# Optimization experiments

Measured on AMD Instinct MI355X. Metric: run time of the kernel, lower is better.

Reference implementation:

```python
import jax, jax.numpy as jnp
import numpy as np

B, N, K, D = 4, 2048, 32, 256
TOKEN_DIM = 256
EGO_DIM = 256
NUM_HEADS = 4
LN_EPS = 1e-6


def masked_softmax(logits, mask, axis):
    mask = mask.astype(jnp.bool_)
    while mask.ndim < logits.ndim:
        mask = mask[..., None]
    neg_big = jnp.finfo(logits.dtype).min
    has_any = jnp.any(mask, axis=axis, keepdims=True)
    masked_logits = jnp.where(mask, logits, neg_big)
    masked_logits = jnp.where(has_any, masked_logits, 0.0)
    weights = jax.nn.softmax(masked_logits, axis=axis)
    weights = jnp.where(mask, weights, 0.0)
    denom = jnp.sum(weights, axis=axis, keepdims=True)
    weights = jnp.where(denom > 0, weights / denom, 0.0)
    return weights


def setup_inputs() -> dict:
    key = jax.random.key(0)
    ks = jax.random.split(key, 10)
    inv_tok = jax.random.normal(ks[0], (B, N, K, D), dtype=jnp.float32)
    ego_ctx = jax.random.normal(ks[1], (B, N, EGO_DIM), dtype=jnp.float32)
    r = jax.random.normal(ks[2], (B, N, K, 3), dtype=jnp.float32)
    u = jax.random.normal(ks[3], (B, N, K, 3), dtype=jnp.float32)
    mask = jax.random.randint(ks[4], (B, N, K), 0, 2).astype(jnp.bool_)
    # params
    W_ego = jax.random.normal(ks[5], (EGO_DIM, TOKEN_DIM), dtype=jnp.float32) * 0.05
    b_ego = jnp.zeros((TOKEN_DIM,), dtype=jnp.float32)
    ln_scale = jnp.ones((D,), dtype=jnp.float32)
    ln_bias = jnp.zeros((D,), dtype=jnp.float32)
    W_h = jax.random.normal(ks[6], (D + TOKEN_DIM, TOKEN_DIM), dtype=jnp.float32) * 0.05
    b_h = jnp.zeros((TOKEN_DIM,), dtype=jnp.float32)
    W_logit = jax.random.normal(ks[7], (TOKEN_DIM, NUM_HEADS), dtype=jnp.float32) * 0.01
    b_logit = jnp.zeros((NUM_HEADS,), dtype=jnp.float32)
    return {"inv_tok": inv_tok, "ego_ctx": ego_ctx, "r": r, "u": u, "mask": mask,
            "W_ego": W_ego, "b_ego": b_ego, "ln_scale": ln_scale, "ln_bias": ln_bias,
            "W_h": W_h, "b_h": b_h, "W_logit": W_logit, "b_logit": b_logit}


def reference(inv_tok, ego_ctx, r, u, mask, W_ego, b_ego, ln_scale, ln_bias, W_h, b_h, W_logit, b_logit):
    # ego context projection, broadcast over K
    ego_h = ego_ctx @ W_ego + b_ego                      # (B,N,T)
    ego_b = jnp.broadcast_to(ego_h[:, :, None, :], (B, N, K, TOKEN_DIM))
    # LayerNorm over last axis of inv_tok
    mean = jnp.mean(inv_tok, axis=-1, keepdims=True)
    var = jnp.var(inv_tok, axis=-1, keepdims=True)
    ln = (inv_tok - mean) * jax.lax.rsqrt(var + LN_EPS) * ln_scale + ln_bias
    h = jnp.concatenate([ln, ego_b], axis=-1)            # (B,N,K,D+T)
    h = jax.nn.gelu(h @ W_h + b_h, approximate=True)     # (B,N,K,T)
    logits = h @ W_logit + b_logit                       # (B,N,K,H)
    alpha = masked_softmax(logits, mask, axis=-2)        # (B,N,K,H)
    v_r = jnp.einsum('bnkh,bnkd->bnhd', alpha, r).reshape(B, N, 3 * NUM_HEADS)
    v_u = jnp.einsum('bnkh,bnkd->bnhd', alpha, u).reshape(B, N, 3 * NUM_HEADS)
    return (v_r, v_u, alpha)
```

## Files before the change

kernel.cpp:

```cpp
#include <hip/hip_runtime.h>

#define BN_TOTAL 8192
#define KTOK 32
#define DDIM 256
#define TDIM 256

typedef float f32x4 __attribute__((ext_vector_type(4)));
typedef short bf16x8 __attribute__((ext_vector_type(8)));

__device__ __forceinline__ unsigned short f2bf(float f){
    unsigned int u = __builtin_bit_cast(unsigned int, f);
    u = u + 0x7fffu + ((u >> 16) & 1u);
    return (unsigned short)(u >> 16);
}
__device__ __forceinline__ float bf2f(unsigned short h){
    unsigned int u = ((unsigned int)h) << 16;
    return __builtin_bit_cast(float, u);
}
__device__ __forceinline__ float gelu_tanh(float x){
    float y = 1.5957691216057308f * (x + 0.044715f * x * x * x);
    return x / (1.0f + __expf(-y));
}

__device__ __forceinline__ int packpos(int k, int n, int NT){
    int kt = k >> 5, quad = (k >> 3) & 3, j = k & 7;
    int nt = n >> 4, nl = n & 15;
    return ((kt * NT + nt) * 64 + quad * 16 + nl) * 8 + j;
}

__global__ __launch_bounds__(256) void pack_weights(const float* __restrict__ Wh,
        const float* __restrict__ Wlogit, const float* __restrict__ b_ego,
        const float* __restrict__ b_h,
        unsigned short* __restrict__ Bp1, unsigned short* __restrict__ BpL,
        float* __restrict__ b_combo){
    int bid = blockIdx.x, tid = threadIdx.x;
    if (bid < 64){
        int base = (bid * 256 + tid) * 4;
        for (int e = base; e < base + 4; ++e){
            int k = e >> 8, n = e & 255;
            Bp1[packpos(k, n, 16)] = f2bf(Wh[k * 256 + n]);
        }
    } else if (bid == 64){
        for (int e = tid * 16; e < tid * 16 + 16; ++e){
            int k = e >> 4, n = e & 15;
            float v = (n < 4) ? Wlogit[k * 4 + n] : 0.0f;
            BpL[packpos(k, n, 1)] = f2bf(v);
        }
    } else {
        float acc = b_h[tid];
        for (int j = 0; j < 256; ++j) acc += b_ego[j] * Wh[(256 + j) * 256 + tid];
        b_combo[tid] = acc;
    }
}

__global__ __launch_bounds__(256) void combo_pack(const float* __restrict__ Wego,
        const float* __restrict__ Wh, unsigned short* __restrict__ Bpc){
    __shared__ float row[256];
    int k = blockIdx.x, n = threadIdx.x;
    row[n] = Wego[k * 256 + n];
    __syncthreads();
    float acc = 0.f;
    const float4* row4 = (const float4*)row;
    for (int j4 = 0; j4 < 64; ++j4){
        float4 e = row4[j4];
        int j = j4 * 4;
        acc += e.x * Wh[(256 + j) * 256 + n];
        acc += e.y * Wh[(257 + j) * 256 + n];
        acc += e.z * Wh[(258 + j) * 256 + n];
        acc += e.w * Wh[(259 + j) * 256 + n];
    }
    Bpc[packpos(k, n, 16)] = f2bf(acc);
}

__global__ __launch_bounds__(256) void ego_gemm(const float* __restrict__ ego_ctx,
        const unsigned short* __restrict__ Bpc, const float* __restrict__ b_combo,
        unsigned short* __restrict__ ego_term){
    int w = threadIdx.x >> 6, l = threadIdx.x & 63;
    int row = blockIdx.x * 64 + w * 16 + (l & 15);
    f32x4 acc[16];
    #pragma unroll
    for (int i = 0; i < 16; ++i) acc[i] = 0;
    #pragma unroll
    for (int kt = 0; kt < 8; ++kt){
        int k0 = kt * 32 + ((l >> 4) << 3);
        const float* ap = ego_ctx + row * 256 + k0;
        float4 x0 = *(const float4*)ap;
        float4 x1 = *(const float4*)(ap + 4);
        bf16x8 a;
        a[0]=(short)f2bf(x0.x); a[1]=(short)f2bf(x0.y); a[2]=(short)f2bf(x0.z); a[3]=(short)f2bf(x0.w);
        a[4]=(short)f2bf(x1.x); a[5]=(short)f2bf(x1.y); a[6]=(short)f2bf(x1.z); a[7]=(short)f2bf(x1.w);
        #pragma unroll
        for (int nt = 0; nt < 16; ++nt){
            bf16x8 b = *(const bf16x8*)&Bpc[((kt * 16 + nt) * 64 + l) * 8];
            acc[nt] = __builtin_amdgcn_mfma_f32_16x16x32_bf16(a, b, acc[nt], 0, 0, 0);
        }
    }
    int rq = (l >> 4) * 4, col = l & 15;
    int rbase = blockIdx.x * 64 + w * 16 + rq;
    #pragma unroll
    for (int nt = 0; nt < 16; ++nt){
        int n = nt * 16 + col;
        float bc = b_combo[n];
        #pragma unroll
        for (int rg = 0; rg < 4; ++rg)
            ego_term[(rbase + rg) * 256 + n] = f2bf(acc[nt][rg] + bc);
    }
}

__global__ __launch_bounds__(256) void main_fused(const float* __restrict__ inv,
        const float* __restrict__ rin, const float* __restrict__ uin,
        const int* __restrict__ mask, const float* __restrict__ ln_s,
        const float* __restrict__ ln_b, const float* __restrict__ b_logit,
        const unsigned short* __restrict__ Bp1, const unsigned short* __restrict__ BpL,
        const unsigned short* __restrict__ ego_term, float* __restrict__ out){

    __shared__ unsigned short Albs[64 * 264];
    __shared__ float ego_s[2][256];
    __shared__ float logit_s[64 * 4];
    __shared__ float alpha_s[64 * 4];

    int tid = threadIdx.x;
    int w = tid >> 6, l = tid & 63;
    int T0 = blockIdx.x * 64;
    int bn0 = blockIdx.x * 2;

    for (int i = tid; i < 512; i += 256)
        ego_s[i >> 8][i & 255] = bf2f(ego_term[bn0 * 256 + i]);

    {
        float4 sc = *(const float4*)&ln_s[l * 4];
        float4 bs = *(const float4*)&ln_b[l * 4];
        int r0 = w * 16;
        const float* base = inv + (T0 + r0) * 256 + l * 4;
        float4 cur = *(const float4*)base;
        #pragma unroll
        for (int rr = 0; rr < 16; ++rr){
            float4 nxt = cur;
            if (rr < 15) nxt = *(const float4*)(base + (rr + 1) * 256);
            float s  = cur.x + cur.y + cur.z + cur.w;
            float s2 = cur.x*cur.x + cur.y*cur.y + cur.z*cur.z + cur.w*cur.w;
            #pragma unroll
            for (int off = 32; off >= 1; off >>= 1){
                s  += __shfl_xor(s,  off);
                s2 += __shfl_xor(s2, off);
            }
            float mean = s * (1.0f / 256.0f);
            float var  = s2 * (1.0f / 256.0f) - mean * mean;
            float rstd = rsqrtf(var + 1e-6f);
            ushort4 o;
            o.x = f2bf((cur.x - mean) * rstd * sc.x + bs.x);
            o.y = f2bf((cur.y - mean) * rstd * sc.y + bs.y);
            o.z = f2bf((cur.z - mean) * rstd * sc.z + bs.z);
            o.w = f2bf((cur.w - mean) * rstd * sc.w + bs.w);
            *(ushort4*)&Albs[(r0 + rr) * 264 + l * 4] = o;
            cur = nxt;
        }
    }
    __syncthreads();

    f32x4 acc[4][4];
    #pragma unroll
    for (int a = 0; a < 4; ++a)
        #pragma unroll
        for (int b = 0; b < 4; ++b) acc[a][b] = 0;
    {
        int kq = (l >> 4) << 3, ml = l & 15;
        #pragma unroll
        for (int kt = 0; kt < 8; ++kt){
            int ko = kt * 32 + kq;
            bf16x8 af[4], bfv[4];
            #pragma unroll
            for (int mt = 0; mt < 4; ++mt)
                af[mt] = *(const bf16x8*)&Albs[(mt * 16 + ml) * 264 + ko];
            #pragma unroll
            for (int i = 0; i < 4; ++i)
                bfv[i] = *(const bf16x8*)&Bp1[((kt * 16 + (w * 4 + i)) * 64 + l) * 8];
            #pragma unroll
            for (int mt = 0; mt < 4; ++mt)
                #pragma unroll
                for (int i = 0; i < 4; ++i)
                    acc[mt][i] = __builtin_amdgcn_mfma_f32_16x16x32_bf16(af[mt], bfv[i], acc[mt][i], 0, 0, 0);
        }
    }
    __syncthreads();

    {
        int col = l & 15, rq = (l >> 4) * 4;
        #pragma unroll
        for (int mt = 0; mt < 4; ++mt){
            int g = mt >> 1;
            #pragma unroll
            for (int i = 0; i < 4; ++i){
                int n = (w * 4 + i) * 16 + col;
                float eg = ego_s[g][n];
                #pragma unroll
                for (int rg = 0; rg < 4; ++rg){
                    float x = acc[mt][i][rg] + eg;
                    Albs[(mt * 16 + rq + rg) * 264 + n] = f2bf(gelu_tanh(x));
                }
            }
        }
    }
    __syncthreads();

    {
        int kq = (l >> 4) << 3, ml = l & 15;
        f32x4 lacc = 0;
        #pragma unroll
        for (int kt = 0; kt < 8; ++kt){
            bf16x8 a = *(const bf16x8*)&Albs[(w * 16 + ml) * 264 + kt * 32 + kq];
            bf16x8 b = *(const bf16x8*)&BpL[(kt * 64 + l) * 8];
            lacc = __builtin_amdgcn_mfma_f32_16x16x32_bf16(a, b, lacc, 0, 0, 0);
        }
        if (ml < 4){
            float bl = b_logit[ml];
            int rq = (l >> 4) * 4;
            #pragma unroll
            for (int rg = 0; rg < 4; ++rg)
                logit_s[(w * 16 + rq + rg) * 4 + ml] = lacc[rg] + bl;
        }
    }
    __syncthreads();

    {
        int g = w >> 1;
        int h = ((w & 1) << 1) + (l >> 5);
        int k = l & 31;
        int valid = mask[T0 + g * 32 + k] != 0;
        float lg = logit_s[(g * 32 + k) * 4 + h];
        float val = valid ? lg : -3.0e38f;
        float mx = val;
        #pragma unroll
        for (int off = 16; off >= 1; off >>= 1)
            mx = fmaxf(mx, __shfl_xor(mx, off));
        float e = valid ? __expf(lg - mx) : 0.0f;
        float ssum = e;
        #pragma unroll
        for (int off = 16; off >= 1; off >>= 1)
            ssum += __shfl_xor(ssum, off);
        float a = (ssum > 0.f) ? e / ssum : 0.0f;
        alpha_s[(g * 32 + k) * 4 + h] = a;
        out[196608 + (T0 + g * 32 + k) * 4 + h] = a;
    }
    __syncthreads();

    if (tid < 48){
        int g = tid / 24, rem = tid % 24;
        int which = rem / 12, hd = rem % 12;
        int h = hd / 3, d = hd % 3;
        const float* src = which ? uin : rin;
        const float* sp = src + (T0 + g * 32) * 3 + d;
        float acc2 = 0.f;
        #pragma unroll
        for (int k = 0; k < 32; ++k)
            acc2 += alpha_s[(g * 32 + k) * 4 + h] * sp[k * 3];
        out[which * 98304 + (bn0 + g) * 12 + hd] = acc2;
    }
}

extern "C" void kernel_launch(void* const* d_in, const int* in_sizes, int n_in,
                              void* d_out, int out_size, void* d_ws, size_t ws_size,
                              hipStream_t stream){
    const float* inv    = (const float*)d_in[0];
    const float* ego    = (const float*)d_in[1];
    const float* rin    = (const float*)d_in[2];
    const float* uin    = (const float*)d_in[3];
    const int*   mask   = (const int*)  d_in[4];
    const float* Wego   = (const float*)d_in[5];
    const float* b_ego  = (const float*)d_in[6];
    const float* ln_s   = (const float*)d_in[7];
    const float* ln_b   = (const float*)d_in[8];
    const float* Wh     = (const float*)d_in[9];
    const float* b_h    = (const float*)d_in[10];
    const float* Wlogit = (const float*)d_in[11];
    const float* b_lg   = (const float*)d_in[12];
    float* out = (float*)d_out;

    unsigned short* wsu = (unsigned short*)d_ws;
    unsigned short* Bp1 = wsu;
    unsigned short* Bpc = wsu + 65536;
    unsigned short* BpL = wsu + 131072;
    float* b_combo      = (float*)(wsu + 135168);
    unsigned short* ego_term = wsu + 135680;

    pack_weights<<<66, 256, 0, stream>>>(Wh, Wlogit, b_ego, b_h, Bp1, BpL, b_combo);
    combo_pack<<<256, 256, 0, stream>>>(Wego, Wh, Bpc);
    ego_gemm<<<128, 256, 0, stream>>>(ego, Bpc, b_combo, ego_term);
    main_fused<<<4096, 256, 0, stream>>>(inv, rin, uin, mask, ln_s, ln_b, b_lg,
                                         Bp1, BpL, ego_term, out);
}
```

Baseline: 473.9 us.

## Fold LayerNorm into GEMM epilogue via MFMA-computed row statistics

LayerNorm is no longer applied before the GEMM. Raw inv_tok is packed to bf16 directly, and the LN scale is folded into the packed Wh weights. The LN bias is folded into the combined bias, and a precomputed column-sum vector v1 handles the mean correction. Per-row sum and sum of squares are produced by extra MFMAs (against a ones vector and against the row itself), and normalisation is applied in the GELU epilogue. This removes the shuffle-reduction pass from the load phase. The prep kernels are merged into one launch, ego_gemm is re-tiled across more blocks, and GELU uses a hardware reciprocal. The cost is precision: statistics come from bf16-rounded inputs and the variance uses the E[x^2]-mean^2 form.

```diff
diff --git a/kernel.cpp b/kernel.cpp
--- a/kernel.cpp
+++ b/kernel.cpp
@@ -1,9 +1,4 @@
 #include <hip/hip_runtime.h>
-
-#define BN_TOTAL 8192
-#define KTOK 32
-#define DDIM 256
-#define TDIM 256
 
 typedef float f32x4 __attribute__((ext_vector_type(4)));
 typedef short bf16x8 __attribute__((ext_vector_type(8)));
@@ -17,9 +12,15 @@
     unsigned int u = ((unsigned int)h) << 16;
     return __builtin_bit_cast(float, u);
 }
-__device__ __forceinline__ float gelu_tanh(float x){
-    float y = 1.5957691216057308f * (x + 0.044715f * x * x * x);
-    return x / (1.0f + __expf(-y));
+__device__ __forceinline__ unsigned int pk2(float a, float b){
+    return (unsigned int)f2bf(a) | ((unsigned int)f2bf(b) << 16);
+}
+__device__ __forceinline__ float gelu_f(float x){
+    float t = x * x;
+    float u = fmaf(0.044715f, t, 1.0f);
+    float y = 1.5957691216057308f * x * u;
+    float e = __expf(-y);
+    return x * __builtin_amdgcn_rcpf(1.0f + e);
 }
 
 __device__ __forceinline__ int packpos(int k, int n, int NT){
@@ -28,17 +29,22 @@
     return ((kt * NT + nt) * 64 + quad * 16 + nl) * 8 + j;
 }
 
-__global__ __launch_bounds__(256) void pack_weights(const float* __restrict__ Wh,
-        const float* __restrict__ Wlogit, const float* __restrict__ b_ego,
-        const float* __restrict__ b_h,
+__global__ __launch_bounds__(256) void prep(const float* __restrict__ Wh,
+        const float* __restrict__ Wlogit, const float* __restrict__ Wego,
+        const float* __restrict__ b_ego, const float* __restrict__ b_h,
+        const float* __restrict__ ln_s, const float* __restrict__ ln_b,
         unsigned short* __restrict__ Bp1, unsigned short* __restrict__ BpL,
-        float* __restrict__ b_combo){
+        unsigned short* __restrict__ Bpc, float* __restrict__ b_combo,
+        float* __restrict__ v1){
+    __shared__ float rowbuf[256];
     int bid = blockIdx.x, tid = threadIdx.x;
     if (bid < 64){
         int base = (bid * 256 + tid) * 4;
+        int k = base >> 8;
+        float sc = ln_s[k];
         for (int e = base; e < base + 4; ++e){
-            int k = e >> 8, n = e & 255;
-            Bp1[packpos(k, n, 16)] = f2bf(Wh[k * 256 + n]);
+            int n = e & 255;
+            Bp1[packpos(k, n, 16)] = f2bf(sc * Wh[k * 256 + n]);
         }
     } else if (bid == 64){
         for (int e = tid * 16; e < tid * 16 + 16; ++e){
@@ -46,157 +52,167 @@
             float v = (n < 4) ? Wlogit[k * 4 + n] : 0.0f;
             BpL[packpos(k, n, 1)] = f2bf(v);
         }
-    } else {
+    } else if (bid == 65){
         float acc = b_h[tid];
         for (int j = 0; j < 256; ++j) acc += b_ego[j] * Wh[(256 + j) * 256 + tid];
+        for (int k = 0; k < 256; ++k) acc += ln_b[k] * Wh[k * 256 + tid];
         b_combo[tid] = acc;
-    }
-}
-
-__global__ __launch_bounds__(256) void combo_pack(const float* __restrict__ Wego,
-        const float* __restrict__ Wh, unsigned short* __restrict__ Bpc){
-    __shared__ float row[256];
-    int k = blockIdx.x, n = threadIdx.x;
-    row[n] = Wego[k * 256 + n];
-    __syncthreads();
-    float acc = 0.f;
-    const float4* row4 = (const float4*)row;
-    for (int j4 = 0; j4 < 64; ++j4){
-        float4 e = row4[j4];
-        int j = j4 * 4;
-        acc += e.x * Wh[(256 + j) * 256 + n];
-        acc += e.y * Wh[(257 + j) * 256 + n];
-        acc += e.z * Wh[(258 + j) * 256 + n];
-        acc += e.w * Wh[(259 + j) * 256 + n];
-    }
-    Bpc[packpos(k, n, 16)] = f2bf(acc);
+    } else if (bid == 66){
+        float acc = 0.f;
+        for (int k = 0; k < 256; ++k)
+            acc += bf2f(f2bf(ln_s[k] * Wh[k * 256 + tid]));
+        v1[tid] = acc;
+    } else {
+        int k = bid - 67;
+        rowbuf[tid] = Wego[k * 256 + tid];
+        __syncthreads();
+        float acc = 0.f;
+        const float4* row4 = (const float4*)rowbuf;
+        for (int j4 = 0; j4 < 64; ++j4){
+            float4 e = row4[j4];
+            int j = j4 * 4;
+            acc += e.x * Wh[(256 + j) * 256 + tid];
+            acc += e.y * Wh[(257 + j) * 256 + tid];
+            acc += e.z * Wh[(258 + j) * 256 + tid];
+            acc += e.w * Wh[(259 + j) * 256 + tid];
+        }
+        Bpc[packpos(k, tid, 16)] = f2bf(acc);
+    }
 }
 
 __global__ __launch_bounds__(256) void ego_gemm(const float* __restrict__ ego_ctx,
         const unsigned short* __restrict__ Bpc, const float* __restrict__ b_combo,
         unsigned short* __restrict__ ego_term){
-    int w = threadIdx.x >> 6, l = threadIdx.x & 63;
-    int row = blockIdx.x * 64 + w * 16 + (l & 15);
-    f32x4 acc[16];
-    #pragma unroll
-    for (int i = 0; i < 16; ++i) acc[i] = 0;
+    const int tid = threadIdx.x, w = tid >> 6, l = tid & 63;
+    const int m0 = blockIdx.x * 16;
+    const int row = m0 + (l & 15);
+    const int kq = (l >> 4) << 3;
+    f32x4 acc[4];
+    #pragma unroll
+    for (int j = 0; j < 4; ++j) acc[j] = 0;
     #pragma unroll
     for (int kt = 0; kt < 8; ++kt){
-        int k0 = kt * 32 + ((l >> 4) << 3);
-        const float* ap = ego_ctx + row * 256 + k0;
+        const float* ap = ego_ctx + row * 256 + kt * 32 + kq;
         float4 x0 = *(const float4*)ap;
         float4 x1 = *(const float4*)(ap + 4);
-        bf16x8 a;
-        a[0]=(short)f2bf(x0.x); a[1]=(short)f2bf(x0.y); a[2]=(short)f2bf(x0.z); a[3]=(short)f2bf(x0.w);
-        a[4]=(short)f2bf(x1.x); a[5]=(short)f2bf(x1.y); a[6]=(short)f2bf(x1.z); a[7]=(short)f2bf(x1.w);
-        #pragma unroll
-        for (int nt = 0; nt < 16; ++nt){
+        uint4 pu = {pk2(x0.x, x0.y), pk2(x0.z, x0.w), pk2(x1.x, x1.y), pk2(x1.z, x1.w)};
+        bf16x8 a = __builtin_bit_cast(bf16x8, pu);
+        #pragma unroll
+        for (int j = 0; j < 4; ++j){
+            int nt = w * 4 + j;
             bf16x8 b = *(const bf16x8*)&Bpc[((kt * 16 + nt) * 64 + l) * 8];
-            acc[nt] = __builtin_amdgcn_mfma_f32_16x16x32_bf16(a, b, acc[nt], 0, 0, 0);
-        }
-    }
-    int rq = (l >> 4) * 4, col = l & 15;
-    int rbase = blockIdx.x * 64 + w * 16 + rq;
-    #pragma unroll
-    for (int nt = 0; nt < 16; ++nt){
-        int n = nt * 16 + col;
+            acc[j] = __builtin_amdgcn_mfma_f32_16x16x32_bf16(a, b, acc[j], 0, 0, 0);
+        }
+    }
+    const int rq = (l >> 4) << 2, colc = l & 15;
+    #pragma unroll
+    for (int j = 0; j < 4; ++j){
+        int n = (w * 4 + j) * 16 + colc;
         float bc = b_combo[n];
         #pragma unroll
         for (int rg = 0; rg < 4; ++rg)
-            ego_term[(rbase + rg) * 256 + n] = f2bf(acc[nt][rg] + bc);
+            ego_term[(m0 + rq + rg) * 256 + n] = f2bf(acc[j][rg] + bc);
     }
 }
 
 __global__ __launch_bounds__(256) void main_fused(const float* __restrict__ inv,
         const float* __restrict__ rin, const float* __restrict__ uin,
-        const int* __restrict__ mask, const float* __restrict__ ln_s,
-        const float* __restrict__ ln_b, const float* __restrict__ b_logit,
+        const int* __restrict__ mask, const float* __restrict__ b_logit,
         const unsigned short* __restrict__ Bp1, const unsigned short* __restrict__ BpL,
-        const unsigned short* __restrict__ ego_term, float* __restrict__ out){
+        const unsigned short* __restrict__ ego_term, const float* __restrict__ v1g,
+        float* __restrict__ out){
 
     __shared__ unsigned short Albs[64 * 264];
-    __shared__ float ego_s[2][256];
-    __shared__ float logit_s[64 * 4];
-    __shared__ float alpha_s[64 * 4];
-
-    int tid = threadIdx.x;
-    int w = tid >> 6, l = tid & 63;
-    int T0 = blockIdx.x * 64;
-    int bn0 = blockIdx.x * 2;
-
-    for (int i = tid; i < 512; i += 256)
-        ego_s[i >> 8][i & 255] = bf2f(ego_term[bn0 * 256 + i]);
+    __shared__ float2 stats_s[64];
+    __shared__ float logit_s[256];
+    __shared__ float alpha_s[256];
+
+    const int tid = threadIdx.x;
+    const int w = tid >> 6, l = tid & 63;
+    const int T0 = blockIdx.x * 64;
+    const int bn0 = blockIdx.x * 2;
+    const int col = l & 15;
+    const int kq = (l >> 4) << 3;
 
     {
-        float4 sc = *(const float4*)&ln_s[l * 4];
-        float4 bs = *(const float4*)&ln_b[l * 4];
-        int r0 = w * 16;
+        const int r0 = w * 16;
         const float* base = inv + (T0 + r0) * 256 + l * 4;
-        float4 cur = *(const float4*)base;
         #pragma unroll
         for (int rr = 0; rr < 16; ++rr){
-            float4 nxt = cur;
-            if (rr < 15) nxt = *(const float4*)(base + (rr + 1) * 256);
-            float s  = cur.x + cur.y + cur.z + cur.w;
-            float s2 = cur.x*cur.x + cur.y*cur.y + cur.z*cur.z + cur.w*cur.w;
-            #pragma unroll
-            for (int off = 32; off >= 1; off >>= 1){
-                s  += __shfl_xor(s,  off);
-                s2 += __shfl_xor(s2, off);
+            float4 c = *(const float4*)(base + rr * 256);
+            uint2 p;
+            p.x = pk2(c.x, c.y);
+            p.y = pk2(c.z, c.w);
+            *(uint2*)&Albs[(r0 + rr) * 264 + l * 4] = p;
+        }
+    }
+    float v1r[4], egv[2][4];
+    #pragma unroll
+    for (int i = 0; i < 4; ++i){
+        int n = w * 64 + i * 16 + col;
+        v1r[i]    = v1g[n];
+        egv[0][i] = bf2f(ego_term[(bn0    ) * 256 + n]);
+        egv[1][i] = bf2f(ego_term[(bn0 + 1) * 256 + n]);
+    }
+    __syncthreads();
+
+    f32x4 acc[4][4];
+    #pragma unroll
+    for (int a = 0; a < 4; ++a)
+        #pragma unroll
+        for (int b = 0; b < 4; ++b) acc[a][b] = 0;
+    f32x4 gacc = 0, sacc = 0;
+    bf16x8 ones;
+    #pragma unroll
+    for (int j = 0; j < 8; ++j) ones[j] = (short)0x3F80;
+
+    #pragma unroll
+    for (int kt = 0; kt < 8; ++kt){
+        const int ko = kt * 32 + kq;
+        bf16x8 af[4], bv[4];
+        #pragma unroll
+        for (int mt = 0; mt < 4; ++mt)
+            af[mt] = *(const bf16x8*)&Albs[(mt * 16 + col) * 264 + ko];
+        #pragma unroll
+        for (int i = 0; i < 4; ++i)
+            bv[i] = *(const bf16x8*)&Bp1[((kt * 16 + (w * 4 + i)) * 64 + l) * 8];
+        #pragma unroll
+        for (int mt = 0; mt < 4; ++mt){
+            if (mt == w){
+                gacc = __builtin_amdgcn_mfma_f32_16x16x32_bf16(af[mt], af[mt], gacc, 0, 0, 0);
+                sacc = __builtin_amdgcn_mfma_f32_16x16x32_bf16(af[mt], ones,   sacc, 0, 0, 0);
             }
-            float mean = s * (1.0f / 256.0f);
-            float var  = s2 * (1.0f / 256.0f) - mean * mean;
-            float rstd = rsqrtf(var + 1e-6f);
-            ushort4 o;
-            o.x = f2bf((cur.x - mean) * rstd * sc.x + bs.x);
-            o.y = f2bf((cur.y - mean) * rstd * sc.y + bs.y);
-            o.z = f2bf((cur.z - mean) * rstd * sc.z + bs.z);
-            o.w = f2bf((cur.w - mean) * rstd * sc.w + bs.w);
-            *(ushort4*)&Albs[(r0 + rr) * 264 + l * 4] = o;
-            cur = nxt;
-        }
-    }
-    __syncthreads();
-
-    f32x4 acc[4][4];
-    #pragma unroll
-    for (int a = 0; a < 4; ++a)
-        #pragma unroll
-        for (int b = 0; b < 4; ++b) acc[a][b] = 0;
-    {
-        int kq = (l >> 4) << 3, ml = l & 15;
-        #pragma unroll
-        for (int kt = 0; kt < 8; ++kt){
-            int ko = kt * 32 + kq;
-            bf16x8 af[4], bfv[4];
-            #pragma unroll
-            for (int mt = 0; mt < 4; ++mt)
-                af[mt] = *(const bf16x8*)&Albs[(mt * 16 + ml) * 264 + ko];
             #pragma unroll
             for (int i = 0; i < 4; ++i)
-                bfv[i] = *(const bf16x8*)&Bp1[((kt * 16 + (w * 4 + i)) * 64 + l) * 8];
+                acc[mt][i] = __builtin_amdgcn_mfma_f32_16x16x32_bf16(af[mt], bv[i], acc[mt][i], 0, 0, 0);
+        }
+    }
+    if ((col >> 2) == (l >> 4)){
+        int rg = col & 3;
+        float mean = sacc[rg] * (1.0f / 256.0f);
+        float var  = gacc[rg] * (1.0f / 256.0f) - mean * mean;
+        float rstd = rsqrtf(var + 1e-6f);
+        stats_s[w * 16 + col] = float2{rstd, rstd * mean};
+    }
+    __syncthreads();
+
+    {
+        const int rq = (l >> 4) << 2;
+        #pragma unroll
+        for (int mt = 0; mt < 4; ++mt){
+            const int g = mt >> 1;
+            float2 st[4];
             #pragma unroll
-            for (int mt = 0; mt < 4; ++mt)
-                #pragma unroll
-                for (int i = 0; i < 4; ++i)
-                    acc[mt][i] = __builtin_amdgcn_mfma_f32_16x16x32_bf16(af[mt], bfv[i], acc[mt][i], 0, 0, 0);
-        }
-    }
-    __syncthreads();
-
-    {
-        int col = l & 15, rq = (l >> 4) * 4;
-        #pragma unroll
-        for (int mt = 0; mt < 4; ++mt){
-            int g = mt >> 1;
+            for (int rg = 0; rg < 4; ++rg) st[rg] = stats_s[mt * 16 + rq + rg];
             #pragma unroll
             for (int i = 0; i < 4; ++i){
-                int n = (w * 4 + i) * 16 + col;
-                float eg = ego_s[g][n];
+                const int n = w * 64 + i * 16 + col;
+                const float base_t = egv[g][i];
                 #pragma unroll
                 for (int rg = 0; rg < 4; ++rg){
-                    float x = acc[mt][i][rg] + eg;
-                    Albs[(mt * 16 + rq + rg) * 264 + n] = f2bf(gelu_tanh(x));
+                    float x = fmaf(st[rg].x, acc[mt][i][rg],
+                                   fmaf(-st[rg].y, v1r[i], base_t));
+                    Albs[(mt * 16 + rq + rg) * 264 + n] = f2bf(gelu_f(x));
                 }
             }
         }
@@ -204,20 +220,19 @@
     __syncthreads();
 
     {
-        int kq = (l >> 4) << 3, ml = l & 15;
         f32x4 lacc = 0;
         #pragma unroll
         for (int kt = 0; kt < 8; ++kt){
-            bf16x8 a = *(const bf16x8*)&Albs[(w * 16 + ml) * 264 + kt * 32 + kq];
+            bf16x8 a = *(const bf16x8*)&Albs[(w * 16 + col) * 264 + kt * 32 + kq];
             bf16x8 b = *(const bf16x8*)&BpL[(kt * 64 + l) * 8];
             lacc = __builtin_amdgcn_mfma_f32_16x16x32_bf16(a, b, lacc, 0, 0, 0);
         }
-        if (ml < 4){
-            float bl = b_logit[ml];
-            int rq = (l >> 4) * 4;
+        if (col < 4){
+            float bl = b_logit[col];
+            const int rq = (l >> 4) << 2;
             #pragma unroll
             for (int rg = 0; rg < 4; ++rg)
-                logit_s[(w * 16 + rq + rg) * 4 + ml] = lacc[rg] + bl;
+                logit_s[(w * 16 + rq + rg) * 4 + col] = lacc[rg] + bl;
         }
     }
     __syncthreads();
@@ -281,11 +296,12 @@
     unsigned short* Bpc = wsu + 65536;
     unsigned short* BpL = wsu + 131072;
     float* b_combo      = (float*)(wsu + 135168);
-    unsigned short* ego_term = wsu + 135680;
-
-    pack_weights<<<66, 256, 0, stream>>>(Wh, Wlogit, b_ego, b_h, Bp1, BpL, b_combo);
-    combo_pack<<<256, 256, 0, stream>>>(Wego, Wh, Bpc);
-    ego_gemm<<<128, 256, 0, stream>>>(ego, Bpc, b_combo, ego_term);
-    main_fused<<<4096, 256, 0, stream>>>(inv, rin, uin, mask, ln_s, ln_b, b_lg,
-                                         Bp1, BpL, ego_term, out);
-}
+    float* v1           = (float*)(wsu + 135680);
+    unsigned short* ego_term = wsu + 136192;
+
+    prep<<<323, 256, 0, stream>>>(Wh, Wlogit, Wego, b_ego, b_h, ln_s, ln_b,
+                                  Bp1, BpL, Bpc, b_combo, v1);
+    ego_gemm<<<512, 256, 0, stream>>>(ego, Bpc, b_combo, ego_term);
+    main_fused<<<4096, 256, 0, stream>>>(inv, rin, uin, mask, b_lg,
+                                         Bp1, BpL, ego_term, v1, out);
+}
```

New measurement: 455.7 us. -3.8%, faster.
